# Performance work log

Measured on AMD Instinct MI355X. Metric: run time of the kernel, lower is better.

## Reference

```python
import jax, jax.numpy as jnp
import numpy as np

IN_DIM = 128
OUT_DIM = 128
HEADS = 4
HEAD_DIM = OUT_DIM // HEADS
N_NODES = 50000
N_EDGES = 800000
NEG_SLOPE = 0.2
LN_EPS = 1e-5


def setup_inputs() -> dict:
    key = jax.random.key(0)
    ks = jax.random.split(key, 10)
    x = jax.random.normal(ks[0], (N_NODES, IN_DIM), dtype=jnp.float32)
    edge_index = jax.random.randint(ks[1], (2, N_EDGES), 0, N_NODES, dtype=jnp.int64)
    s = 1.0 / np.sqrt(IN_DIM)
    W_l = jax.random.normal(ks[2], (IN_DIM, HEADS * HEAD_DIM), dtype=jnp.float32) * s
    b_l = jnp.zeros((HEADS * HEAD_DIM,), dtype=jnp.float32)
    W_r = jax.random.normal(ks[3], (IN_DIM, HEADS * HEAD_DIM), dtype=jnp.float32) * s
    b_r = jnp.zeros((HEADS * HEAD_DIM,), dtype=jnp.float32)
    att = jax.random.normal(ks[4], (HEADS, HEAD_DIM), dtype=jnp.float32) * (1.0 / np.sqrt(HEAD_DIM))
    bias = jnp.zeros((HEADS * HEAD_DIM,), dtype=jnp.float32)
    gamma = jnp.ones((OUT_DIM,), dtype=jnp.float32)
    beta = jnp.zeros((OUT_DIM,), dtype=jnp.float32)
    return {"x": x, "edge_index": edge_index, "W_l": W_l, "b_l": b_l,
            "W_r": W_r, "b_r": b_r, "att": att, "bias": bias,
            "gamma": gamma, "beta": beta}


def reference(x, edge_index, W_l, b_l, W_r, b_r, att, bias, gamma, beta):
    N = x.shape[0]
    src, dst = edge_index[0], edge_index[1]
    # GATv2: separate linear transforms for source and target nodes
    xl = (x @ W_l + b_l).reshape(N, HEADS, HEAD_DIM)  # source / message features
    xr = (x @ W_r + b_r).reshape(N, HEADS, HEAD_DIM)  # target features
    # per-edge attention logits: a^T . leaky_relu(xl[src] + xr[dst])  -> [E, H]
    h = jax.nn.leaky_relu(xl[src] + xr[dst], NEG_SLOPE)
    e = jnp.einsum('ehd,hd->eh', h, att)
    # segment softmax over edges grouped by destination node
    m = jax.ops.segment_max(e, dst, num_segments=N)
    m = jnp.where(jnp.isfinite(m), m, 0.0)  # guard empty segments
    ex = jnp.exp(e - m[dst])
    denom = jax.ops.segment_sum(ex, dst, num_segments=N)
    alpha = ex / (denom[dst] + 1e-16)  # [E, H]
    # scatter-add weighted source features (dropout omitted: eval mode)
    out = jax.ops.segment_sum(alpha[:, :, None] * xl[src], dst, num_segments=N)
    out = out.reshape(N, HEADS * HEAD_DIM) + bias
    # residual (in_dim == out_dim) + LayerNorm
    out = out + x
    mu = out.mean(axis=-1, keepdims=True)
    var = ((out - mu) ** 2).mean(axis=-1, keepdims=True)
    return (out - mu) * jax.lax.rsqrt(var + LN_EPS) * gamma + beta
```

## Files before the change

kernel.cpp:

```cpp
#include <hip/hip_runtime.h>
#include <math.h>

#define NEG_SLOPE 0.2f
#define LN_EPS 1e-5f
#define CAP 64
#define HB 4096
#define RUN 56
#define XSTR 136
#define SMEM_BYTES (64 * XSTR * 2)

typedef __attribute__((ext_vector_type(8))) short s8v;
typedef __attribute__((ext_vector_type(8))) unsigned short u8v;
typedef __attribute__((ext_vector_type(4))) float f4v;
typedef _Float16 h2 __attribute__((ext_vector_type(2)));

__device__ inline unsigned short f2bf(float f) {
    unsigned u = __float_as_uint(f);
    return (unsigned short)((u + 0x7FFFu + ((u >> 16) & 1u)) >> 16);
}

__global__ __launch_bounds__(256) void pre_scat_kernel(
    const int* __restrict__ src, const int* __restrict__ dst,
    const float* __restrict__ Wl, const float* __restrict__ Wr,
    unsigned short* __restrict__ packL, unsigned short* __restrict__ packR,
    unsigned* __restrict__ part, int* __restrict__ cntmat,
    int E, int NBKT) {
    const int bid = blockIdx.x, tid = threadIdx.x;
    if (bid < 2) {
        const float* W = bid ? Wr : Wl;
        unsigned short* pk = bid ? packR : packL;
        #pragma unroll
        for (int it = 0; it < 16; ++it) {
            int pos4 = tid + it * 256;
            int k = pos4 >> 5, c4 = pos4 & 31;
            float4 v = *(const float4*)&W[k * 128 + c4 * 4];
            int t = k >> 5, lane_hi = (k & 31) >> 3, j = k & 7;
            float vv[4] = {v.x, v.y, v.z, v.w};
            #pragma unroll
            for (int u = 0; u < 4; ++u) {
                int n = c4 * 4 + u;
                int idx = ((((n >> 4) * 4 + t) * 64) + lane_hi * 16 + (n & 15)) * 8 + j;
                pk[idx] = f2bf(vv[u]);
            }
        }
        return;
    }
    __shared__ int cnt[256];
    const int sb = bid - 2;
    const int e0 = sb * HB;
    cnt[tid] = 0;
    __syncthreads();
    for (int j = tid; j < HB; j += 256) {
        int e = e0 + j;
        if (e < E) {
            int d = dst[e];
            int b = d >> 8;
            int r = atomicAdd(&cnt[b], 1);
            if (r < RUN)
                part[((size_t)sb * NBKT + b) * RUN + r] =
                    ((unsigned)(d & 255) << 16) | (unsigned)src[e];
        }
    }
    __syncthreads();
    if (tid < NBKT) {
        int c = cnt[tid]; if (c > RUN) c = RUN;
        cntmat[(size_t)sb * NBKT + tid] = c;
    }
}

__global__ __launch_bounds__(256, 4) void fill_tf_kernel(
    const unsigned* __restrict__ part, const int* __restrict__ cntmat,
    unsigned short* __restrict__ csr, int* __restrict__ deg,
    const float* __restrict__ x,
    const unsigned short* __restrict__ packL, const unsigned short* __restrict__ packR,
    const float* __restrict__ bl, const float* __restrict__ br,
    _Float16* __restrict__ xl, _Float16* __restrict__ xr,
    int N, int NBKT, int NSC) {
    const int bid = blockIdx.x, tid = threadIdx.x;
    __shared__ __align__(16) char smem[SMEM_BYTES];

    if (bid < NBKT) {
        int* cur = (int*)smem;
        cur[tid] = 0;
        __syncthreads();
        const int b = bid;
        if (tid < NSC) {
            int cnt = cntmat[(size_t)tid * NBKT + b];
            const unsigned* seg = part + ((size_t)tid * NBKT + b) * RUN;
            for (int i = 0; i < cnt; ++i) {
                unsigned rec = seg[i];
                int dl = rec >> 16;
                int pos = atomicAdd(&cur[dl], 1);
                if (pos < CAP)
                    csr[(size_t)(b * 256 + dl) * CAP + (((pos & 3) << 4) | (pos >> 2))] =
                        (unsigned short)(rec & 0xFFFFu);
            }
        }
        __syncthreads();
        int node = b * 256 + tid;
        if (node < N) {
            int dgc = cur[tid]; if (dgc > CAP) dgc = CAP;
            deg[node] = dgc;
            int dgp = (dgc + 3) & ~3; if (dgp > CAP) dgp = CAP;
            for (int p = dgc; p < dgp; ++p)
                csr[(size_t)node * CAP + (((p & 3) << 4) | (p >> 2))] = (unsigned short)node;
        }
        return;
    }

    unsigned short* xs = (unsigned short*)smem;
    const int tb = bid - NBKT;
    const int blk0 = tb * 64;

    #pragma unroll
    for (int it = 0; it < 8; ++it) {
        int slot = tid + it * 256;
        int row = slot >> 5, c4 = slot & 31;
        int node = blk0 + row;
        float4 v = make_float4(0.f, 0.f, 0.f, 0.f);
        if (node < N) v = *(const float4*)&x[(size_t)node * 128 + 4 * c4];
        ushort4 o;
        o.x = f2bf(v.x); o.y = f2bf(v.y); o.z = f2bf(v.z); o.w = f2bf(v.w);
        *(ushort4*)&xs[row * XSTR + 4 * c4] = o;
    }
    __syncthreads();

    const int wv = tid >> 6, lane = tid & 63;
    const int row = lane & 15, q = lane >> 4;

    s8v afrag[4];
    #pragma unroll
    for (int t = 0; t < 4; ++t)
        afrag[t] = *(const s8v*)&xs[(wv * 16 + row) * XSTR + t * 32 + q * 8];

    __syncthreads();
    _Float16* ys = (_Float16*)smem;

    #pragma unroll 1
    for (int side = 0; side < 2; ++side) {
        const unsigned short* __restrict__ pk = side ? packR : packL;
        const float* __restrict__ bb = side ? br : bl;
        _Float16* __restrict__ dsth = side ? xr : xl;

        f4v acc[8];
        #pragma unroll
        for (int nt = 0; nt < 8; ++nt) acc[nt] = (f4v){0.f, 0.f, 0.f, 0.f};

        #pragma unroll
        for (int t = 0; t < 4; ++t) {
            #pragma unroll
            for (int np = 0; np < 2; ++np) {
                s8v bfr[4];
                #pragma unroll
                for (int u = 0; u < 4; ++u)
                    bfr[u] = *(const s8v*)&pk[(((np * 4 + u) * 4 + t) * 64 + lane) * 8];
                #pragma unroll
                for (int u = 0; u < 4; ++u)
                    acc[np * 4 + u] = __builtin_amdgcn_mfma_f32_16x16x32_bf16(
                        afrag[t], bfr[u], acc[np * 4 + u], 0, 0, 0);
            }
        }

        #pragma unroll
        for (int nt = 0; nt < 8; ++nt) {
            float bcol = bb[nt * 16 + row];
            #pragma unroll
            for (int r2 = 0; r2 < 4; ++r2)
                ys[(wv * 16 + q * 4 + r2) * XSTR + nt * 16 + row] =
                    (_Float16)(acc[nt][r2] + bcol);
        }
        __syncthreads();
        #pragma unroll
        for (int it = 0; it < 4; ++it) {
            int slot = tid + it * 256;
            int rrow = slot >> 4, c8 = slot & 15;
            int nd = blk0 + rrow;
            if (nd < N)
                *(float4*)&dsth[(size_t)nd * 128 + c8 * 8] =
                    *(const float4*)&ys[rrow * XSTR + c8 * 8];
        }
        __syncthreads();
    }
}

__device__ inline void edge_body(float4 raw, const h2* xr2, const h2* av2,
                                 h2 ns2, bool valid, float& den, float* acc) {
    h2 c[4];
    c[0] = __builtin_bit_cast(h2, raw.x);
    c[1] = __builtin_bit_cast(h2, raw.y);
    c[2] = __builtin_bit_cast(h2, raw.z);
    c[3] = __builtin_bit_cast(h2, raw.w);
    float p = 0.f;
    #pragma unroll
    for (int j = 0; j < 4; ++j) {
        h2 t = c[j] + xr2[j];
        h2 hh = __builtin_elementwise_max(t, t * ns2);
#if __has_builtin(__builtin_amdgcn_fdot2)
        p = __builtin_amdgcn_fdot2(hh, av2[j], p, false);
#else
        p = fmaf((float)hh.x, (float)av2[j].x, p);
        p = fmaf((float)hh.y, (float)av2[j].y, p);
#endif
    }
    p += __shfl_xor(p, 1);
    p += __shfl_xor(p, 2);
    float w = __expf(p);
    w = valid ? w : 0.f;
    den += w;
    #pragma unroll
    for (int j = 0; j < 4; ++j) {
        acc[2 * j]     = fmaf(w, (float)c[j].x, acc[2 * j]);
        acc[2 * j + 1] = fmaf(w, (float)c[j].y, acc[2 * j + 1]);
    }
}

__global__ __launch_bounds__(1024) void gat_kernel(
    const int* __restrict__ deg_arr, const unsigned short* __restrict__ csr,
    const _Float16* __restrict__ xl, const _Float16* __restrict__ xr,
    const float* __restrict__ att, const float* __restrict__ x,
    const float* __restrict__ bias, const float* __restrict__ gamma,
    const float* __restrict__ beta, float* __restrict__ out, int N) {
    const int node = blockIdx.x * 16 + (threadIdx.x >> 6);
    const int lane = threadIdx.x & 63;
    if (node >= N) return;
    const int sub = lane & 15;
    const int eg  = lane >> 4;
    const int f0  = sub * 8;

    int dg = deg_arr[node]; if (dg > CAP) dg = CAP;
    int kmax = (dg + 3) >> 2; if (kmax > 8) kmax = 8;
    kmax = __builtin_amdgcn_readfirstlane(kmax);

    const unsigned short* crow = csr + (size_t)node * CAP;
    u8v cidx = *(const u8v*)&crow[eg * 16];

    float4 bufv[8];
    #pragma unroll
    for (int k = 0; k < 8; ++k)
        if (k < kmax) bufv[k] = *(const float4*)&xl[(size_t)(unsigned short)cidx[k] * 128 + f0];

    h2 xr2[4], av2[4];
    {
        float4 xrw = *(const float4*)&xr[(size_t)node * 128 + f0];
        float fw[4]; fw[0] = xrw.x; fw[1] = xrw.y; fw[2] = xrw.z; fw[3] = xrw.w;
        #pragma unroll
        for (int j = 0; j < 4; ++j) xr2[j] = __builtin_bit_cast(h2, fw[j]);
        float4 c0 = *(const float4*)&att[f0];
        float4 c1 = *(const float4*)&att[f0 + 4];
        av2[0] = (h2){(_Float16)c0.x, (_Float16)c0.y};
        av2[1] = (h2){(_Float16)c0.z, (_Float16)c0.w};
        av2[2] = (h2){(_Float16)c1.x, (_Float16)c1.y};
        av2[3] = (h2){(_Float16)c1.z, (_Float16)c1.w};
    }
    const h2 ns2 = (h2){(_Float16)NEG_SLOPE, (_Float16)NEG_SLOPE};

    float den0 = 0.f, den1 = 0.f;
    float a0[8] = {0,0,0,0,0,0,0,0}, a1[8] = {0,0,0,0,0,0,0,0};

    #pragma unroll
    for (int k = 0; k < 8; k += 2) {
        if (k < kmax)     edge_body(bufv[k],     xr2, av2, ns2, eg + 4 * k < dg, den0, a0);
        if (k + 1 < kmax) edge_body(bufv[k + 1], xr2, av2, ns2, eg + 4 * (k + 1) < dg, den1, a1);
    }

    if (dg > 32) {
        u8v cidx2 = *(const u8v*)&crow[eg * 16 + 8];
        #pragma unroll
        for (int k = 0; k < 8; ++k) {
            int i = eg + 32 + 4 * k;
            if (i < dg) {
                float4 raw = *(const float4*)&xl[(size_t)(unsigned short)cidx2[k] * 128 + f0];
                edge_body(raw, xr2, av2, ns2, true, (k & 1) ? den1 : den0, (k & 1) ? a1 : a0);
            }
        }
    }

    float den = den0 + den1;
    float acc[8];
    #pragma unroll
    for (int j = 0; j < 8; ++j) acc[j] = a0[j] + a1[j];

    den += __shfl_xor(den, 16); den += __shfl_xor(den, 32);
    #pragma unroll
    for (int j = 0; j < 8; ++j) {
        acc[j] += __shfl_xor(acc[j], 16);
        acc[j] += __shfl_xor(acc[j], 32);
    }

    const float inv = 1.0f / (den + 1e-16f);
    float v[8];
    {
        float4 b0 = *(const float4*)&bias[f0];
        float4 b1 = *(const float4*)&bias[f0 + 4];
        float4 r0 = *(const float4*)&x[(size_t)node * 128 + f0];
        float4 r1 = *(const float4*)&x[(size_t)node * 128 + f0 + 4];
        const float bbf[8] = {b0.x, b0.y, b0.z, b0.w, b1.x, b1.y, b1.z, b1.w};
        const float rrf[8] = {r0.x, r0.y, r0.z, r0.w, r1.x, r1.y, r1.z, r1.w};
        #pragma unroll
        for (int j = 0; j < 8; ++j) v[j] = acc[j] * inv + bbf[j] + rrf[j];
    }

    float s = v[0] + v[1] + v[2] + v[3] + v[4] + v[5] + v[6] + v[7];
    s += __shfl_xor(s, 1); s += __shfl_xor(s, 2);
    s += __shfl_xor(s, 4); s += __shfl_xor(s, 8);
    const float mu = s * (1.0f / 128.0f);

    float d[8], vs = 0.f;
    #pragma unroll
    for (int j = 0; j < 8; ++j) { d[j] = v[j] - mu; vs = fmaf(d[j], d[j], vs); }
    vs += __shfl_xor(vs, 1); vs += __shfl_xor(vs, 2);
    vs += __shfl_xor(vs, 4); vs += __shfl_xor(vs, 8);
    const float rstd = rsqrtf(vs * (1.0f / 128.0f) + LN_EPS);

    if (eg == 0) {
        float4 g0 = *(const float4*)&gamma[f0];
        float4 g1 = *(const float4*)&gamma[f0 + 4];
        float4 e0 = *(const float4*)&beta[f0];
        float4 e1 = *(const float4*)&beta[f0 + 4];
        float4 o0, o1;
        o0.x = d[0] * rstd * g0.x + e0.x;  o0.y = d[1] * rstd * g0.y + e0.y;
        o0.z = d[2] * rstd * g0.z + e0.z;  o0.w = d[3] * rstd * g0.w + e0.w;
        o1.x = d[4] * rstd * g1.x + e1.x;  o1.y = d[5] * rstd * g1.y + e1.y;
        o1.z = d[6] * rstd * g1.z + e1.z;  o1.w = d[7] * rstd * g1.w + e1.w;
        *(float4*)&out[(size_t)node * 128 + f0]     = o0;
        *(float4*)&out[(size_t)node * 128 + f0 + 4] = o1;
    }
}

extern "C" void kernel_launch(void* const* d_in, const int* in_sizes, int n_in,
                              void* d_out, int out_size, void* d_ws, size_t ws_size,
                              hipStream_t stream) {
    const float* x     = (const float*)d_in[0];
    const int*   ei    = (const int*)d_in[1];
    const float* Wl    = (const float*)d_in[2];
    const float* bl    = (const float*)d_in[3];
    const float* Wr    = (const float*)d_in[4];
    const float* br    = (const float*)d_in[5];
    const float* att   = (const float*)d_in[6];
    const float* bias  = (const float*)d_in[7];
    const float* gamma = (const float*)d_in[8];
    const float* beta  = (const float*)d_in[9];

    const int N = in_sizes[0] / 128;
    const int E = in_sizes[1] / 2;
    const int* src = ei;
    const int* dst = ei + E;

    const int NBKT = (N + 255) >> 8;
    const int NSC  = (E + HB - 1) / HB;
    const int TBS  = (N + 63) / 64;

    char* w = (char*)d_ws;
    _Float16*       xl    = (_Float16*)w;        w += (size_t)N * 128 * sizeof(_Float16);
    _Float16*       xr    = (_Float16*)w;        w += (size_t)N * 128 * sizeof(_Float16);
    unsigned short* packL = (unsigned short*)w;  w += 16384 * sizeof(unsigned short);
    unsigned short* packR = (unsigned short*)w;  w += 16384 * sizeof(unsigned short);
    unsigned*       part  = (unsigned*)w;        w += (size_t)NSC * NBKT * RUN * sizeof(unsigned);
    int*            cntmat= (int*)w;             w += (size_t)NSC * NBKT * sizeof(int);
    unsigned short* csr   = (unsigned short*)w;  w += (size_t)N * CAP * sizeof(unsigned short);
    int*            deg   = (int*)w;             w += (size_t)N * sizeof(int);

    pre_scat_kernel<<<2 + NSC, 256, 0, stream>>>(
        src, dst, Wl, Wr, packL, packR, part, cntmat, E, NBKT);
    fill_tf_kernel<<<NBKT + TBS, 256, 0, stream>>>(
        part, cntmat, csr, deg, x, packL, packR, bl, br, xl, xr, N, NBKT, NSC);
    gat_kernel<<<(N + 15) / 16, 1024, 0, stream>>>(
        deg, csr, xl, xr, att, x, bias, gamma, beta, (float*)d_out, N);
}
```

Measured before the change: 186.3 us.

## Process node pairs per wave in a persistent grid-stride GAT kernel

The GAT aggregation kernel becomes a persistent grid-stride kernel of 2048 blocks of 256 threads. Each wave handles two destination nodes and issues both nodes' neighbor gathers before computing, to raise memory-level parallelism. CSR padding to a multiple of 4 and the per-edge valid mask are removed, and edges are instead guarded by per-lane degree checks. The two partial accumulators are merged into one, which shortens register pressure but also shortens the independent FMA chains. Twice as many gather buffers per wave may raise register use and lower occupancy.

```diff
diff --git a/kernel.cpp b/kernel.cpp
--- a/kernel.cpp
+++ b/kernel.cpp
@@ -98,13 +98,7 @@
         }
         __syncthreads();
         int node = b * 256 + tid;
-        if (node < N) {
-            int dgc = cur[tid]; if (dgc > CAP) dgc = CAP;
-            deg[node] = dgc;
-            int dgp = (dgc + 3) & ~3; if (dgp > CAP) dgp = CAP;
-            for (int p = dgc; p < dgp; ++p)
-                csr[(size_t)node * CAP + (((p & 3) << 4) | (p >> 2))] = (unsigned short)node;
-        }
+        if (node < N) deg[node] = cur[tid];
         return;
     }
 
@@ -184,7 +178,7 @@
 }
 
 __device__ inline void edge_body(float4 raw, const h2* xr2, const h2* av2,
-                                 h2 ns2, bool valid, float& den, float* acc) {
+                                 h2 ns2, float& den, float* acc) {
     h2 c[4];
     c[0] = __builtin_bit_cast(h2, raw.x);
     c[1] = __builtin_bit_cast(h2, raw.y);
@@ -205,7 +199,6 @@
     p += __shfl_xor(p, 1);
     p += __shfl_xor(p, 2);
     float w = __expf(p);
-    w = valid ? w : 0.f;
     den += w;
     #pragma unroll
     for (int j = 0; j < 4; ++j) {
@@ -214,54 +207,29 @@
     }
 }
 
-__global__ __launch_bounds__(1024) void gat_kernel(
-    const int* __restrict__ deg_arr, const unsigned short* __restrict__ csr,
-    const _Float16* __restrict__ xl, const _Float16* __restrict__ xr,
-    const float* __restrict__ att, const float* __restrict__ x,
-    const float* __restrict__ bias, const float* __restrict__ gamma,
-    const float* __restrict__ beta, float* __restrict__ out, int N) {
-    const int node = blockIdx.x * 16 + (threadIdx.x >> 6);
-    const int lane = threadIdx.x & 63;
-    if (node >= N) return;
+__device__ inline void gat_node(
+    int node, int dg, int lane, const float4* bufv, float4 xrw,
+    const unsigned short* crow, const _Float16* __restrict__ xl,
+    const h2* av2, h2 ns2,
+    const float* __restrict__ bias, const float* __restrict__ x,
+    const float* __restrict__ gamma, const float* __restrict__ beta,
+    float* __restrict__ out) {
     const int sub = lane & 15;
     const int eg  = lane >> 4;
     const int f0  = sub * 8;
 
-    int dg = deg_arr[node]; if (dg > CAP) dg = CAP;
-    int kmax = (dg + 3) >> 2; if (kmax > 8) kmax = 8;
-    kmax = __builtin_amdgcn_readfirstlane(kmax);
-
-    const unsigned short* crow = csr + (size_t)node * CAP;
-    u8v cidx = *(const u8v*)&crow[eg * 16];
-
-    float4 bufv[8];
+    h2 xr2[4];
+    {
+        float fw[4]; fw[0] = xrw.x; fw[1] = xrw.y; fw[2] = xrw.z; fw[3] = xrw.w;
+        #pragma unroll
+        for (int j = 0; j < 4; ++j) xr2[j] = __builtin_bit_cast(h2, fw[j]);
+    }
+
+    float den = 0.f;
+    float acc[8] = {0,0,0,0,0,0,0,0};
     #pragma unroll
     for (int k = 0; k < 8; ++k)
-        if (k < kmax) bufv[k] = *(const float4*)&xl[(size_t)(unsigned short)cidx[k] * 128 + f0];
-
-    h2 xr2[4], av2[4];
-    {
-        float4 xrw = *(const float4*)&xr[(size_t)node * 128 + f0];
-        float fw[4]; fw[0] = xrw.x; fw[1] = xrw.y; fw[2] = xrw.z; fw[3] = xrw.w;
-        #pragma unroll
-        for (int j = 0; j < 4; ++j) xr2[j] = __builtin_bit_cast(h2, fw[j]);
-        float4 c0 = *(const float4*)&att[f0];
-        float4 c1 = *(const float4*)&att[f0 + 4];
-        av2[0] = (h2){(_Float16)c0.x, (_Float16)c0.y};
-        av2[1] = (h2){(_Float16)c0.z, (_Float16)c0.w};
-        av2[2] = (h2){(_Float16)c1.x, (_Float16)c1.y};
-        av2[3] = (h2){(_Float16)c1.z, (_Float16)c1.w};
-    }
-    const h2 ns2 = (h2){(_Float16)NEG_SLOPE, (_Float16)NEG_SLOPE};
-
-    float den0 = 0.f, den1 = 0.f;
-    float a0[8] = {0,0,0,0,0,0,0,0}, a1[8] = {0,0,0,0,0,0,0,0};
-
-    #pragma unroll
-    for (int k = 0; k < 8; k += 2) {
-        if (k < kmax)     edge_body(bufv[k],     xr2, av2, ns2, eg + 4 * k < dg, den0, a0);
-        if (k + 1 < kmax) edge_body(bufv[k + 1], xr2, av2, ns2, eg + 4 * (k + 1) < dg, den1, a1);
-    }
+        if (eg + 4 * k < dg) edge_body(bufv[k], xr2, av2, ns2, den, acc);
 
     if (dg > 32) {
         u8v cidx2 = *(const u8v*)&crow[eg * 16 + 8];
@@ -270,15 +238,10 @@
             int i = eg + 32 + 4 * k;
             if (i < dg) {
                 float4 raw = *(const float4*)&xl[(size_t)(unsigned short)cidx2[k] * 128 + f0];
-                edge_body(raw, xr2, av2, ns2, true, (k & 1) ? den1 : den0, (k & 1) ? a1 : a0);
+                edge_body(raw, xr2, av2, ns2, den, acc);
             }
         }
     }
-
-    float den = den0 + den1;
-    float acc[8];
-    #pragma unroll
-    for (int j = 0; j < 8; ++j) acc[j] = a0[j] + a1[j];
 
     den += __shfl_xor(den, 16); den += __shfl_xor(den, 32);
     #pragma unroll
@@ -324,6 +287,63 @@
         o1.z = d[6] * rstd * g1.z + e1.z;  o1.w = d[7] * rstd * g1.w + e1.w;
         *(float4*)&out[(size_t)node * 128 + f0]     = o0;
         *(float4*)&out[(size_t)node * 128 + f0 + 4] = o1;
+    }
+}
+
+__global__ __launch_bounds__(256) void gat_kernel(
+    const int* __restrict__ deg_arr, const unsigned short* __restrict__ csr,
+    const _Float16* __restrict__ xl, const _Float16* __restrict__ xr,
+    const float* __restrict__ att, const float* __restrict__ x,
+    const float* __restrict__ bias, const float* __restrict__ gamma,
+    const float* __restrict__ beta, float* __restrict__ out,
+    int N, int NPAIR, int NWAVES) {
+    const int lane = threadIdx.x & 63;
+    const int gw = blockIdx.x * 4 + (threadIdx.x >> 6);
+    const int sub = lane & 15;
+    const int eg  = lane >> 4;
+    const int f0  = sub * 8;
+
+    h2 av2[4];
+    {
+        float4 c0 = *(const float4*)&att[f0];
+        float4 c1 = *(const float4*)&att[f0 + 4];
+        av2[0] = (h2){(_Float16)c0.x, (_Float16)c0.y};
+        av2[1] = (h2){(_Float16)c0.z, (_Float16)c0.w};
+        av2[2] = (h2){(_Float16)c1.x, (_Float16)c1.y};
+        av2[3] = (h2){(_Float16)c1.z, (_Float16)c1.w};
+    }
+    const h2 ns2 = (h2){(_Float16)NEG_SLOPE, (_Float16)NEG_SLOPE};
+
+    for (int p = gw; p < NPAIR; p += NWAVES) {
+        const int nA = 2 * p, nB = 2 * p + 1;
+        const bool hasB = nB < N;
+
+        int dgA = deg_arr[nA]; if (dgA > CAP) dgA = CAP;
+        int dgB = hasB ? deg_arr[nB] : 0; if (dgB > CAP) dgB = CAP;
+        const unsigned short* crA = csr + (size_t)nA * CAP;
+        const unsigned short* crB = csr + (size_t)nB * CAP;
+        u8v cidxA = *(const u8v*)&crA[eg * 16];
+        u8v cidxB = (u8v){0,0,0,0,0,0,0,0};
+        if (hasB) cidxB = *(const u8v*)&crB[eg * 16];
+        float4 xrwA = *(const float4*)&xr[(size_t)nA * 128 + f0];
+        float4 xrwB = make_float4(0.f, 0.f, 0.f, 0.f);
+        if (hasB) xrwB = *(const float4*)&xr[(size_t)nB * 128 + f0];
+
+        float4 bufA[8], bufB[8];
+        #pragma unroll
+        for (int k = 0; k < 8; ++k) {
+            int i = eg + 4 * k;
+            if (i < dgA) bufA[k] = *(const float4*)&xl[(size_t)(unsigned short)cidxA[k] * 128 + f0];
+        }
+        #pragma unroll
+        for (int k = 0; k < 8; ++k) {
+            int i = eg + 4 * k;
+            if (i < dgB) bufB[k] = *(const float4*)&xl[(size_t)(unsigned short)cidxB[k] * 128 + f0];
+        }
+
+        gat_node(nA, dgA, lane, bufA, xrwA, crA, xl, av2, ns2, bias, x, gamma, beta, out);
+        if (hasB)
+            gat_node(nB, dgB, lane, bufB, xrwB, crB, xl, av2, ns2, bias, x, gamma, beta, out);
     }
 }
 
@@ -349,6 +369,9 @@
     const int NBKT = (N + 255) >> 8;
     const int NSC  = (E + HB - 1) / HB;
     const int TBS  = (N + 63) / 64;
+    const int NPAIR = (N + 1) / 2;
+    const int GATB  = 2048;
+    const int NWAVES = GATB * 4;
 
     char* w = (char*)d_ws;
     _Float16*       xl    = (_Float16*)w;        w += (size_t)N * 128 * sizeof(_Float16);
@@ -364,6 +387,6 @@
         src, dst, Wl, Wr, packL, packR, part, cntmat, E, NBKT);
     fill_tf_kernel<<<NBKT + TBS, 256, 0, stream>>>(
         part, cntmat, csr, deg, x, packL, packR, bl, br, xl, xr, N, NBKT, NSC);
-    gat_kernel<<<(N + 15) / 16, 1024, 0, stream>>>(
-        deg, csr, xl, xr, att, x, bias, gamma, beta, (float*)d_out, N);
-}
+    gat_kernel<<<GATB, 256, 0, stream>>>(
+        deg, csr, xl, xr, att, x, bias, gamma, beta, (float*)d_out, N, NPAIR, NWAVES);
+}
```

Measured after the change: 184.9 us. No clear change (-0.8%).
